# Performance work log

Measured on AMD Instinct MI355X. Metric: run time of the kernel, lower is better.

The kernel has to match this reference:

```python
import jax, jax.numpy as jnp
import numpy as np

B, N, NB, C, CZ = 4, 1024, 32, 384, 128
EPS = 1e-6


def setup_inputs() -> dict:
    key = jax.random.key(0)
    k1, k2, k3, k4, k5 = jax.random.split(key, 5)
    s_i = jax.random.normal(k1, (B, N, C), dtype=jnp.float32)
    s_ij = jax.random.normal(k2, (B, N, NB, C), dtype=jnp.float32)
    m_ij = jnp.ones((B, N, NB), dtype=jnp.float32)
    z_ij = jax.random.normal(k3, (B, N, NB, CZ), dtype=jnp.float32)
    W_s = jax.random.normal(k4, (C, C), dtype=jnp.float32) / np.sqrt(C)
    W_z = jax.random.normal(k5, (CZ, C), dtype=jnp.float32) / np.sqrt(CZ)
    gamma = jnp.ones((C,), dtype=jnp.float32)
    beta = jnp.zeros((C,), dtype=jnp.float32)
    return {"s_i": s_i, "s_ij": s_ij, "m_ij": m_ij, "z_ij": z_ij,
            "W_s": W_s, "W_z": W_z, "gamma": gamma, "beta": beta}


def reference(s_i, s_ij, m_ij, z_ij, W_s, W_z, gamma, beta):
    # Dense projection of neighbor single act: (B,N,n,C) @ (C,C)
    s_proj = jnp.einsum('bnkc,cd->bnkd', s_ij, W_s)
    # subtract center single act
    diff = s_proj - s_i[..., None, :]
    # gate by projected pair act: (B,N,n,Cz) @ (Cz,C)
    gate = jnp.einsum('bnkz,zd->bnkd', z_ij, W_z)
    msg = diff * gate
    # masked sum over neighbor axis
    s_new = jnp.sum(msg * m_ij[..., None], axis=-2)  # (B,N,C)
    # layernorm over last axis
    mu = jnp.mean(s_new, axis=-1, keepdims=True)
    var = jnp.mean(jnp.square(s_new - mu), axis=-1, keepdims=True)
    s_new = (s_new - mu) * jax.lax.rsqrt(var + EPS) * gamma + beta
    return s_new
```

## Files before the change

kernel.cpp:

```cpp
#include <hip/hip_runtime.h>
#include <hip/hip_bf16.h>

#define B_ 4
#define N_ 1024
#define NB_ 32
#define C_ 384
#define CZ_ 128
#define NSITES (B_ * N_)
#define EPSV 1e-6f
#define PAD 40
#define SPB 2
#define MR 64
#define THREADS 512

typedef unsigned short u16;
typedef unsigned int u32;
typedef __bf16 bf16x8 __attribute__((ext_vector_type(8)));
typedef float f32x4 __attribute__((ext_vector_type(4)));

__device__ __forceinline__ u16 f2bf(float f) {
    return __builtin_bit_cast(u16, __float2bfloat16(f));
}
__device__ __forceinline__ u32 pk2(float lo, float hi) {
    return ((u32)f2bf(hi) << 16) | f2bf(lo);
}
__device__ __forceinline__ float bfbits2f(u16 u) {
    union { float f; u32 i; } x;
    x.i = ((u32)u) << 16;
    return x.f;
}

__global__ void prep_weights(const float* __restrict__ Ws, const float* __restrict__ Wz,
                             u16* __restrict__ Wts, u16* __restrict__ Wtz) {
    int idx = blockIdx.x * 256 + threadIdx.x;
    if (idx < C_ * C_) {
        int d = idx / C_, c = idx % C_;
        Wts[idx] = f2bf(Ws[c * C_ + d]);
    } else {
        int j = idx - C_ * C_;
        if (j < C_ * CZ_) {
            int d = j / CZ_, z = j % CZ_;
            Wtz[j] = f2bf(Wz[z * C_ + d]);
        }
    }
}

__global__ __launch_bounds__(THREADS, 4)
void fused_msg_kernel(const float* __restrict__ s_i,
                      const float* __restrict__ s_ij,
                      const float* __restrict__ m_ij,
                      const float* __restrict__ z_ij,
                      const u16* __restrict__ Wts,
                      const u16* __restrict__ Wtz,
                      const float* __restrict__ gamma,
                      const float* __restrict__ beta,
                      float* __restrict__ out) {
    __shared__ u16 ldsW[2][C_ * PAD];
    __shared__ u16 ldsA[2][MR * PAD];
    __shared__ float lds_snew[SPB * C_];

    const int tid = threadIdx.x;
    const int wave = tid >> 6;
    const int lane = tid & 63;
    const int q = lane >> 4;
    const int ln = lane & 15;
    const int mg = wave >> 2;
    const int cb = (wave & 3) * 96;

    const int site0 = blockIdx.x * SPB;
    const long rowbase = (long)site0 * NB_;

    const int arow = tid >> 3, aseg = tid & 7;
    const int wrow = tid >> 2, wseg = tid & 3;
    const int la_w = arow * PAD + aseg * 4;
    const int lw_w = wrow * PAD + wseg * 8;

    const float mv = m_ij[rowbase + lane];

    const f32x4 ZERO = {0.f, 0.f, 0.f, 0.f};
    f32x4 acc[2][6];
    #pragma unroll
    for (int mt = 0; mt < 2; ++mt)
        #pragma unroll
        for (int nt = 0; nt < 6; ++nt)
            acc[mt][nt] = ZERO;

    float4 ra;
    uint4 rw0, rw1, rw2;

    {
        const int kd = CZ_;
        const float* ap = z_ij + (rowbase + arow) * kd + aseg * 4;
        const u16* wp = Wtz + wrow * kd + wseg * 8;
        const int ws1 = 128 * kd, ws2 = 256 * kd;

        ra = *reinterpret_cast<const float4*>(ap);
        rw0 = *reinterpret_cast<const uint4*>(wp);
        rw1 = *reinterpret_cast<const uint4*>(wp + ws1);
        rw2 = *reinterpret_cast<const uint4*>(wp + ws2);
        ap += 32; wp += 32;
        {
            uint2 a2 = {pk2(ra.x, ra.y), pk2(ra.z, ra.w)};
            *reinterpret_cast<uint2*>(&ldsA[0][la_w]) = a2;
            *reinterpret_cast<uint4*>(&ldsW[0][lw_w]) = rw0;
            *reinterpret_cast<uint4*>(&ldsW[0][lw_w + 128 * PAD]) = rw1;
            *reinterpret_cast<uint4*>(&ldsW[0][lw_w + 256 * PAD]) = rw2;
        }
        __syncthreads();

        #pragma unroll 2
        for (int c = 0; c < 4; ++c) {
            if (c + 1 < 4) {
                ra = *reinterpret_cast<const float4*>(ap);
                rw0 = *reinterpret_cast<const uint4*>(wp);
                rw1 = *reinterpret_cast<const uint4*>(wp + ws1);
                rw2 = *reinterpret_cast<const uint4*>(wp + ws2);
                ap += 32; wp += 32;
            }
            const u16* lA = ldsA[c & 1];
            const u16* lW = ldsW[c & 1];
            bf16x8 a0 = *reinterpret_cast<const bf16x8*>(&lA[(mg * 32 + ln) * PAD + q * 8]);
            bf16x8 a1 = *reinterpret_cast<const bf16x8*>(&lA[(mg * 32 + 16 + ln) * PAD + q * 8]);
            #pragma unroll
            for (int nt = 0; nt < 6; ++nt) {
                bf16x8 b = *reinterpret_cast<const bf16x8*>(&lW[(cb + nt * 16 + ln) * PAD + q * 8]);
                acc[0][nt] = __builtin_amdgcn_mfma_f32_16x16x32_bf16(a0, b, acc[0][nt], 0, 0, 0);
                acc[1][nt] = __builtin_amdgcn_mfma_f32_16x16x32_bf16(a1, b, acc[1][nt], 0, 0, 0);
            }
            if (c + 1 < 4) {
                int nb = (c + 1) & 1;
                uint2 a2 = {pk2(ra.x, ra.y), pk2(ra.z, ra.w)};
                *reinterpret_cast<uint2*>(&ldsA[nb][la_w]) = a2;
                *reinterpret_cast<uint4*>(&ldsW[nb][lw_w]) = rw0;
                *reinterpret_cast<uint4*>(&ldsW[nb][lw_w + 128 * PAD]) = rw1;
                *reinterpret_cast<uint4*>(&ldsW[nb][lw_w + 256 * PAD]) = rw2;
            }
            __syncthreads();
        }
    }

    u32 gateb[2][6][2];
    #pragma unroll
    for (int mt = 0; mt < 2; ++mt) {
        int rb = mg * 32 + mt * 16 + q * 4;
        float m0 = __shfl(mv, rb + 0, 64);
        float m1 = __shfl(mv, rb + 1, 64);
        float m2 = __shfl(mv, rb + 2, 64);
        float m3 = __shfl(mv, rb + 3, 64);
        #pragma unroll
        for (int nt = 0; nt < 6; ++nt) {
            gateb[mt][nt][0] = pk2(acc[mt][nt][0] * m0, acc[mt][nt][1] * m1);
            gateb[mt][nt][1] = pk2(acc[mt][nt][2] * m2, acc[mt][nt][3] * m3);
            acc[mt][nt] = ZERO;
        }
    }

    {
        const int kd = C_;
        const float* ap = s_ij + (rowbase + arow) * kd + aseg * 4;
        const u16* wp = Wts + wrow * kd + wseg * 8;
        const int ws1 = 128 * kd, ws2 = 256 * kd;

        ra = *reinterpret_cast<const float4*>(ap);
        rw0 = *reinterpret_cast<const uint4*>(wp);
        rw1 = *reinterpret_cast<const uint4*>(wp + ws1);
        rw2 = *reinterpret_cast<const uint4*>(wp + ws2);
        ap += 32; wp += 32;
        {
            uint2 a2 = {pk2(ra.x, ra.y), pk2(ra.z, ra.w)};
            *reinterpret_cast<uint2*>(&ldsA[0][la_w]) = a2;
            *reinterpret_cast<uint4*>(&ldsW[0][lw_w]) = rw0;
            *reinterpret_cast<uint4*>(&ldsW[0][lw_w + 128 * PAD]) = rw1;
            *reinterpret_cast<uint4*>(&ldsW[0][lw_w + 256 * PAD]) = rw2;
        }
        __syncthreads();

        #pragma unroll 2
        for (int c = 0; c < 12; ++c) {
            if (c + 1 < 12) {
                ra = *reinterpret_cast<const float4*>(ap);
                rw0 = *reinterpret_cast<const uint4*>(wp);
                rw1 = *reinterpret_cast<const uint4*>(wp + ws1);
                rw2 = *reinterpret_cast<const uint4*>(wp + ws2);
                ap += 32; wp += 32;
            }
            const u16* lA = ldsA[c & 1];
            const u16* lW = ldsW[c & 1];
            bf16x8 a0 = *reinterpret_cast<const bf16x8*>(&lA[(mg * 32 + ln) * PAD + q * 8]);
            bf16x8 a1 = *reinterpret_cast<const bf16x8*>(&lA[(mg * 32 + 16 + ln) * PAD + q * 8]);
            #pragma unroll
            for (int nt = 0; nt < 6; ++nt) {
                bf16x8 b = *reinterpret_cast<const bf16x8*>(&lW[(cb + nt * 16 + ln) * PAD + q * 8]);
                acc[0][nt] = __builtin_amdgcn_mfma_f32_16x16x32_bf16(a0, b, acc[0][nt], 0, 0, 0);
                acc[1][nt] = __builtin_amdgcn_mfma_f32_16x16x32_bf16(a1, b, acc[1][nt], 0, 0, 0);
            }
            if (c + 1 < 12) {
                int nb = (c + 1) & 1;
                uint2 a2 = {pk2(ra.x, ra.y), pk2(ra.z, ra.w)};
                *reinterpret_cast<uint2*>(&ldsA[nb][la_w]) = a2;
                *reinterpret_cast<uint4*>(&ldsW[nb][lw_w]) = rw0;
                *reinterpret_cast<uint4*>(&ldsW[nb][lw_w + 128 * PAD]) = rw1;
                *reinterpret_cast<uint4*>(&ldsW[nb][lw_w + 256 * PAD]) = rw2;
            }
            __syncthreads();
        }
    }

    #pragma unroll
    for (int nt = 0; nt < 6; ++nt) {
        int col = cb + nt * 16 + ln;
        float si = s_i[(long)(site0 + mg) * C_ + col];
        float p = 0.f;
        #pragma unroll
        for (int mt = 0; mt < 2; ++mt) {
            #pragma unroll
            for (int r = 0; r < 4; ++r) {
                float g = bfbits2f((u16)(gateb[mt][nt][r >> 1] >> ((r & 1) * 16)));
                p += (acc[mt][nt][r] - si) * g;
            }
        }
        p += __shfl_xor(p, 16, 64);
        p += __shfl_xor(p, 32, 64);
        if (q == 0) lds_snew[mg * C_ + col] = p;
    }
    __syncthreads();

    if (wave < SPB) {
        const int site = wave;
        float v[6];
        float sum = 0.f, sumsq = 0.f;
        #pragma unroll
        for (int i = 0; i < 6; ++i) {
            v[i] = lds_snew[site * C_ + lane + i * 64];
            sum += v[i];
            sumsq += v[i] * v[i];
        }
        #pragma unroll
        for (int off = 32; off >= 1; off >>= 1) {
            sum += __shfl_xor(sum, off, 64);
            sumsq += __shfl_xor(sumsq, off, 64);
        }
        float mu = sum * (1.f / C_);
        float var = sumsq * (1.f / C_) - mu * mu;
        float rs = rsqrtf(var + EPSV);
        #pragma unroll
        for (int i = 0; i < 6; ++i) {
            int col = lane + i * 64;
            out[(long)(site0 + site) * C_ + col] = (v[i] - mu) * rs * gamma[col] + beta[col];
        }
    }
}

extern "C" void kernel_launch(void* const* d_in, const int* in_sizes, int n_in,
                              void* d_out, int out_size, void* d_ws, size_t ws_size,
                              hipStream_t stream) {
    (void)in_sizes; (void)n_in; (void)out_size; (void)ws_size;
    const float* s_i   = (const float*)d_in[0];
    const float* s_ij  = (const float*)d_in[1];
    const float* m_ij  = (const float*)d_in[2];
    const float* z_ij  = (const float*)d_in[3];
    const float* W_s   = (const float*)d_in[4];
    const float* W_z   = (const float*)d_in[5];
    const float* gamma = (const float*)d_in[6];
    const float* beta  = (const float*)d_in[7];
    float* out = (float*)d_out;

    u16* wts = (u16*)d_ws;
    u16* wtz = wts + C_ * C_;

    int prep_elems = C_ * C_ + C_ * CZ_;
    prep_weights<<<(prep_elems + 255) / 256, 256, 0, stream>>>(W_s, W_z, wts, wtz);
    fused_msg_kernel<<<NSITES / SPB, THREADS, 0, stream>>>(s_i, s_ij, m_ij, z_ij, wts, wtz,
                                                           gamma, beta, out);
}
```

Before: 438.7 us.

## Load weight fragments directly from global into registers, drop LDS weight staging

```diff
diff --git a/kernel.cpp b/kernel.cpp
--- a/kernel.cpp
+++ b/kernel.cpp
@@ -55,7 +55,6 @@
                       const float* __restrict__ gamma,
                       const float* __restrict__ beta,
                       float* __restrict__ out) {
-    __shared__ u16 ldsW[2][C_ * PAD];
     __shared__ u16 ldsA[2][MR * PAD];
     __shared__ float lds_snew[SPB * C_];
 
@@ -71,9 +70,7 @@
     const long rowbase = (long)site0 * NB_;
 
     const int arow = tid >> 3, aseg = tid & 7;
-    const int wrow = tid >> 2, wseg = tid & 3;
     const int la_w = arow * PAD + aseg * 4;
-    const int lw_w = wrow * PAD + wseg * 8;
 
     const float mv = m_ij[rowbase + lane];
 
@@ -86,55 +83,36 @@
             acc[mt][nt] = ZERO;
 
     float4 ra;
-    uint4 rw0, rw1, rw2;
 
     {
         const int kd = CZ_;
         const float* ap = z_ij + (rowbase + arow) * kd + aseg * 4;
-        const u16* wp = Wtz + wrow * kd + wseg * 8;
-        const int ws1 = 128 * kd, ws2 = 256 * kd;
+        const u16* wb = Wtz + (cb + ln) * kd + q * 8;
 
         ra = *reinterpret_cast<const float4*>(ap);
-        rw0 = *reinterpret_cast<const uint4*>(wp);
-        rw1 = *reinterpret_cast<const uint4*>(wp + ws1);
-        rw2 = *reinterpret_cast<const uint4*>(wp + ws2);
-        ap += 32; wp += 32;
-        {
-            uint2 a2 = {pk2(ra.x, ra.y), pk2(ra.z, ra.w)};
-            *reinterpret_cast<uint2*>(&ldsA[0][la_w]) = a2;
-            *reinterpret_cast<uint4*>(&ldsW[0][lw_w]) = rw0;
-            *reinterpret_cast<uint4*>(&ldsW[0][lw_w + 128 * PAD]) = rw1;
-            *reinterpret_cast<uint4*>(&ldsW[0][lw_w + 256 * PAD]) = rw2;
-        }
+        ap += 32;
+        *reinterpret_cast<uint2*>(&ldsA[0][la_w]) = uint2{pk2(ra.x, ra.y), pk2(ra.z, ra.w)};
         __syncthreads();
 
-        #pragma unroll 2
+        #pragma unroll 1
         for (int c = 0; c < 4; ++c) {
-            if (c + 1 < 4) {
-                ra = *reinterpret_cast<const float4*>(ap);
-                rw0 = *reinterpret_cast<const uint4*>(wp);
-                rw1 = *reinterpret_cast<const uint4*>(wp + ws1);
-                rw2 = *reinterpret_cast<const uint4*>(wp + ws2);
-                ap += 32; wp += 32;
-            }
+            if (c + 1 < 4) { ra = *reinterpret_cast<const float4*>(ap); ap += 32; }
             const u16* lA = ldsA[c & 1];
-            const u16* lW = ldsW[c & 1];
             bf16x8 a0 = *reinterpret_cast<const bf16x8*>(&lA[(mg * 32 + ln) * PAD + q * 8]);
             bf16x8 a1 = *reinterpret_cast<const bf16x8*>(&lA[(mg * 32 + 16 + ln) * PAD + q * 8]);
+            bf16x8 b[6];
+            #pragma unroll
+            for (int nt = 0; nt < 6; ++nt)
+                b[nt] = *reinterpret_cast<const bf16x8*>(wb + nt * 16 * kd);
+            wb += 32;
             #pragma unroll
             for (int nt = 0; nt < 6; ++nt) {
-                bf16x8 b = *reinterpret_cast<const bf16x8*>(&lW[(cb + nt * 16 + ln) * PAD + q * 8]);
-                acc[0][nt] = __builtin_amdgcn_mfma_f32_16x16x32_bf16(a0, b, acc[0][nt], 0, 0, 0);
-                acc[1][nt] = __builtin_amdgcn_mfma_f32_16x16x32_bf16(a1, b, acc[1][nt], 0, 0, 0);
+                acc[0][nt] = __builtin_amdgcn_mfma_f32_16x16x32_bf16(a0, b[nt], acc[0][nt], 0, 0, 0);
+                acc[1][nt] = __builtin_amdgcn_mfma_f32_16x16x32_bf16(a1, b[nt], acc[1][nt], 0, 0, 0);
             }
-            if (c + 1 < 4) {
-                int nb = (c + 1) & 1;
-                uint2 a2 = {pk2(ra.x, ra.y), pk2(ra.z, ra.w)};
-                *reinterpret_cast<uint2*>(&ldsA[nb][la_w]) = a2;
-                *reinterpret_cast<uint4*>(&ldsW[nb][lw_w]) = rw0;
-                *reinterpret_cast<uint4*>(&ldsW[nb][lw_w + 128 * PAD]) = rw1;
-                *reinterpret_cast<uint4*>(&ldsW[nb][lw_w + 256 * PAD]) = rw2;
-            }
+            if (c + 1 < 4)
+                *reinterpret_cast<uint2*>(&ldsA[(c + 1) & 1][la_w]) =
+                    uint2{pk2(ra.x, ra.y), pk2(ra.z, ra.w)};
             __syncthreads();
         }
     }
@@ -158,50 +136,32 @@
     {
         const int kd = C_;
         const float* ap = s_ij + (rowbase + arow) * kd + aseg * 4;
-        const u16* wp = Wts + wrow * kd + wseg * 8;
-        const int ws1 = 128 * kd, ws2 = 256 * kd;
+        const u16* wb = Wts + (cb + ln) * kd + q * 8;
 
         ra = *reinterpret_cast<const float4*>(ap);
-        rw0 = *reinterpret_cast<const uint4*>(wp);
-        rw1 = *reinterpret_cast<const uint4*>(wp + ws1);
-        rw2 = *reinterpret_cast<const uint4*>(wp + ws2);
-        ap += 32; wp += 32;
-        {
-            uint2 a2 = {pk2(ra.x, ra.y), pk2(ra.z, ra.w)};
-            *reinterpret_cast<uint2*>(&ldsA[0][la_w]) = a2;
-            *reinterpret_cast<uint4*>(&ldsW[0][lw_w]) = rw0;
-            *reinterpret_cast<uint4*>(&ldsW[0][lw_w + 128 * PAD]) = rw1;
-            *reinterpret_cast<uint4*>(&ldsW[0][lw_w + 256 * PAD]) = rw2;
-        }
+        ap += 32;
+        *reinterpret_cast<uint2*>(&ldsA[0][la_w]) = uint2{pk2(ra.x, ra.y), pk2(ra.z, ra.w)};
         __syncthreads();
 
-        #pragma unroll 2
+        #pragma unroll 1
         for (int c = 0; c < 12; ++c) {
-            if (c + 1 < 12) {
-                ra = *reinterpret_cast<const float4*>(ap);
-                rw0 = *reinterpret_cast<const uint4*>(wp);
-                rw1 = *reinterpret_cast<const uint4*>(wp + ws1);
-                rw2 = *reinterpret_cast<const uint4*>(wp + ws2);
-                ap += 32; wp += 32;
-            }
+            if (c + 1 < 12) { ra = *reinterpret_cast<const float4*>(ap); ap += 32; }
             const u16* lA = ldsA[c & 1];
-            const u16* lW = ldsW[c & 1];
             bf16x8 a0 = *reinterpret_cast<const bf16x8*>(&lA[(mg * 32 + ln) * PAD + q * 8]);
             bf16x8 a1 = *reinterpret_cast<const bf16x8*>(&lA[(mg * 32 + 16 + ln) * PAD + q * 8]);
+            bf16x8 b[6];
+            #pragma unroll
+            for (int nt = 0; nt < 6; ++nt)
+                b[nt] = *reinterpret_cast<const bf16x8*>(wb + nt * 16 * kd);
+            wb += 32;
             #pragma unroll
             for (int nt = 0; nt < 6; ++nt) {
-                bf16x8 b = *reinterpret_cast<const bf16x8*>(&lW[(cb + nt * 16 + ln) * PAD + q * 8]);
-                acc[0][nt] = __builtin_amdgcn_mfma_f32_16x16x32_bf16(a0, b, acc[0][nt], 0, 0, 0);
-                acc[1][nt] = __builtin_amdgcn_mfma_f32_16x16x32_bf16(a1, b, acc[1][nt], 0, 0, 0);
+                acc[0][nt] = __builtin_amdgcn_mfma_f32_16x16x32_bf16(a0, b[nt], acc[0][nt], 0, 0, 0);
+                acc[1][nt] = __builtin_amdgcn_mfma_f32_16x16x32_bf16(a1, b[nt], acc[1][nt], 0, 0, 0);
             }
-            if (c + 1 < 12) {
-                int nb = (c + 1) & 1;
-                uint2 a2 = {pk2(ra.x, ra.y), pk2(ra.z, ra.w)};
-                *reinterpret_cast<uint2*>(&ldsA[nb][la_w]) = a2;
-                *reinterpret_cast<uint4*>(&ldsW[nb][lw_w]) = rw0;
-                *reinterpret_cast<uint4*>(&ldsW[nb][lw_w + 128 * PAD]) = rw1;
-                *reinterpret_cast<uint4*>(&ldsW[nb][lw_w + 256 * PAD]) = rw2;
-            }
+            if (c + 1 < 12)
+                *reinterpret_cast<uint2*>(&ldsA[(c + 1) & 1][la_w]) =
+                    uint2{pk2(ra.x, ra.y), pk2(ra.z, ra.w)};
             __syncthreads();
         }
     }
```

Result: slower. 501.5 us (+14.3%).
